# Kernel optimization log

Measured on AMD Instinct MI355X. Metric: run time of the kernel, lower is better.

## Reference

```python
import jax, jax.numpy as jnp
import numpy as np

ALPHA = 0.5      # dendritic temporal decay
BETA = 0.5       # somatic (LIF) decay
V_TH = 1.0
V_RESET = 0.0
N_COMP = 4       # B, dendritic compartments
SG_ALPHA = 4.0   # spikingjelly surrogate.Sigmoid default alpha


def mexican_hat(x, var=0.75, eps=1e-5):
    v = var + eps
    g = jnp.exp(-0.5 * x * x / v) / jnp.sqrt(2.0 * jnp.pi * v)
    return (1.0 - x * x / v) * g / v


@jax.custom_vjp
def heaviside_sg(x):
    # spikingjelly surrogate.Sigmoid: heaviside forward, sigmoid-derivative backward
    return (x >= 0.0).astype(x.dtype)

def _hs_fwd(x):
    return heaviside_sg(x), x

def _hs_bwd(x, g):
    s = jax.nn.sigmoid(SG_ALPHA * x)
    return (g * SG_ALPHA * s * (1.0 - s),)

heaviside_sg.defvjp(_hs_fwd, _hs_bwd)


def setup_inputs() -> dict:
    key = jax.random.key(0)
    k1, _ = jax.random.split(key)
    x_seq = jax.random.normal(k1, (8, 16, 128, 32, 32), dtype=jnp.float32)
    k = jnp.ones((1, N_COMP, 1), dtype=jnp.float32)  # dendritic strength param
    return {"x_seq": x_seq, "k": k}


def reference(x_seq, k):
    T, N, C, H, W = x_seq.shape
    B = N_COMP
    K = C // B
    L = H * W
    x = x_seq.reshape(T, N, K, B, L)

    # lower-triangular alpha decay matrix: A[i, j] = alpha**(i-j) for j <= i
    idx = jnp.arange(T)
    d = idx[:, None] - idx[None, :]
    A = jnp.where(d >= 0, ALPHA ** jnp.maximum(d, 0).astype(x.dtype),
                  jnp.zeros((), x.dtype)).astype(x.dtype)

    # causal alpha-weighted temporal sum (same math as dense broadcast+sum)
    pre_act = jnp.einsum('ts,snkbl->tnkbl', A, x)  # [T,N,K,B,L]

    fs = jax.nn.softmax(k, axis=1)                  # [1,B,1], normalized strength
    y_seq = (fs * 3.0 * mexican_hat(pre_act)).sum(axis=3)  # [T,N,K,L]

    # LIF soma recurrence with hard reset
    def step(h, y_t):
        h = BETA * h + y_t
        spike = heaviside_sg(h - V_TH)
        h = (1.0 - spike) * h + spike * V_RESET
        return h, spike

    h0 = jnp.zeros((N, K, L), dtype=x.dtype)
    _, spike_seq = jax.lax.scan(step, h0, y_seq)    # [T,N,K,L]
    return spike_seq.reshape(T, N, K, H, W)
```

## Files before the change

### kernel.cpp

```cpp
#include <hip/hip_runtime.h>


#define TT 8
#define NB 16
#define CC 128
#define BB 4
#define KK 32
#define LL 1024

__global__ __launch_bounds__(256) void dendsn_fwd(
    const float* __restrict__ x, const float* __restrict__ k,
    float* __restrict__ out)
{
    const int gid = blockIdx.x * 256 + threadIdx.x;
    const int l4 = gid & 255;
    const int kk = (gid >> 8) & 31;
    const int n  = gid >> 13;

    const float k0 = k[0], k1 = k[1], k2 = k[2], k3 = k[3];
    const float m  = fmaxf(fmaxf(k0, k1), fmaxf(k2, k3));
    const float e0 = expf(k0 - m), e1 = expf(k1 - m),
                e2 = expf(k2 - m), e3 = expf(k3 - m);
    const float inv_s = 1.0f / (e0 + e1 + e2 + e3);
    const float fs[4] = { 3.0f * e0 * inv_s, 3.0f * e1 * inv_s,
                          3.0f * e2 * inv_s, 3.0f * e3 * inv_s };

    const float v     = 0.75f + 1e-5f;
    const float inv_v = 1.0f / v;
    const float gs    = 1.0f / sqrtf(2.0f * 3.14159265358979323846f * v);

    const size_t tstride_x = (size_t)NB * CC * LL;
    const size_t tstride_o = (size_t)NB * KK * LL;
    const size_t base_x = ((size_t)n * CC + (size_t)kk * BB) * LL + (size_t)l4 * 4;
    const size_t base_o = ((size_t)n * KK + kk) * LL + (size_t)l4 * 4;

    float pre[4][4];
    float h[4];
    #pragma unroll
    for (int b = 0; b < 4; ++b)
        #pragma unroll
        for (int j = 0; j < 4; ++j) pre[b][j] = 0.0f;
    #pragma unroll
    for (int j = 0; j < 4; ++j) h[j] = 0.0f;

    for (int t = 0; t < TT; ++t) {
        float4 xv[4];
        #pragma unroll
        for (int b = 0; b < 4; ++b)
            xv[b] = *reinterpret_cast<const float4*>(
                        x + base_x + (size_t)t * tstride_x + (size_t)b * LL);

        float y[4] = {0.0f, 0.0f, 0.0f, 0.0f};
        #pragma unroll
        for (int b = 0; b < 4; ++b) {
            const float xs[4] = { xv[b].x, xv[b].y, xv[b].z, xv[b].w };
            #pragma unroll
            for (int j = 0; j < 4; ++j) {
                const float p = 0.5f * pre[b][j] + xs[j];
                pre[b][j] = p;
                const float q = p * p * inv_v;
                const float g = expf(-0.5f * q) * gs;
                y[j] += fs[b] * ((1.0f - q) * g * inv_v);
            }
        }

        float4 o;
        float* op = &o.x;
        #pragma unroll
        for (int j = 0; j < 4; ++j) {
            const float hh = 0.5f * h[j] + y[j];
            const float s  = (hh - 1.0f >= 0.0f) ? 1.0f : 0.0f;
            h[j] = (s != 0.0f) ? 0.0f : hh;
            op[j] = s;
        }
        *reinterpret_cast<float4*>(out + base_o + (size_t)t * tstride_o) = o;
    }
}

extern "C" void kernel_launch(void* const* d_in, const int* in_sizes, int n_in,
                              void* d_out, int out_size, void* d_ws, size_t ws_size,
                              hipStream_t stream)
{
    const float* x = (const float*)d_in[0];
    const float* k = (const float*)d_in[1];
    float* out = (float*)d_out;

    dendsn_fwd<<<512, 256, 0, stream>>>(x, k, out);
}
```

Measured before the change: 21.71 us.

## Split dendritic compartments across wave halves with shuffle reduction and prefetch

Each output quad is now handled by two lanes of a wavefront, each covering two of the four compartments, and the partial sums are combined with a cross-half shuffle. This doubles the thread count and the grid size, giving more waves in flight for a memory-bound kernel. It also software-prefetches the next timestep's inputs, fully unrolls the time loop and adds an occupancy hint to launch bounds. The cost is redundant LIF arithmetic in both halves, the shuffles, and only half of the lanes doing stores.

```diff
diff --git a/kernel.cpp b/kernel.cpp
--- a/kernel.cpp
+++ b/kernel.cpp
@@ -8,22 +8,30 @@
 #define KK 32
 #define LL 1024
 
-__global__ __launch_bounds__(256) void dendsn_fwd(
+__global__ __launch_bounds__(256, 4) void dendsn_fwd(
     const float* __restrict__ x, const float* __restrict__ k,
     float* __restrict__ out)
 {
-    const int gid = blockIdx.x * 256 + threadIdx.x;
-    const int l4 = gid & 255;
-    const int kk = (gid >> 8) & 31;
-    const int n  = gid >> 13;
+    const int tid  = threadIdx.x;
+    const int lane = tid & 63;
+    const int wv   = tid >> 6;
+    const int half = lane >> 5;
+    const int sl   = lane & 31;
+
+    const int pairIdx = (blockIdx.x * 4 + wv) * 32 + sl;
+    const int l4 = pairIdx & 255;
+    const int kk = (pairIdx >> 8) & 31;
+    const int n  = pairIdx >> 13;
+    const int b0 = half * 2;
 
     const float k0 = k[0], k1 = k[1], k2 = k[2], k3 = k[3];
     const float m  = fmaxf(fmaxf(k0, k1), fmaxf(k2, k3));
     const float e0 = expf(k0 - m), e1 = expf(k1 - m),
                 e2 = expf(k2 - m), e3 = expf(k3 - m);
     const float inv_s = 1.0f / (e0 + e1 + e2 + e3);
-    const float fs[4] = { 3.0f * e0 * inv_s, 3.0f * e1 * inv_s,
-                          3.0f * e2 * inv_s, 3.0f * e3 * inv_s };
+    const float fsa[4] = { 3.0f * e0 * inv_s, 3.0f * e1 * inv_s,
+                           3.0f * e2 * inv_s, 3.0f * e3 * inv_s };
+    const float fs0 = fsa[b0], fs1 = fsa[b0 + 1];
 
     const float v     = 0.75f + 1e-5f;
     const float inv_v = 1.0f / v;
@@ -31,38 +39,51 @@
 
     const size_t tstride_x = (size_t)NB * CC * LL;
     const size_t tstride_o = (size_t)NB * KK * LL;
-    const size_t base_x = ((size_t)n * CC + (size_t)kk * BB) * LL + (size_t)l4 * 4;
+    const size_t base_x = ((size_t)n * CC + (size_t)kk * BB + b0) * LL
+                        + (size_t)l4 * 4;
     const size_t base_o = ((size_t)n * KK + kk) * LL + (size_t)l4 * 4;
 
-    float pre[4][4];
+    float pre[2][4];
     float h[4];
     #pragma unroll
-    for (int b = 0; b < 4; ++b)
+    for (int b = 0; b < 2; ++b)
         #pragma unroll
         for (int j = 0; j < 4; ++j) pre[b][j] = 0.0f;
     #pragma unroll
     for (int j = 0; j < 4; ++j) h[j] = 0.0f;
 
+    float4 xv[2], xn[2];
+    xv[0] = *reinterpret_cast<const float4*>(x + base_x);
+    xv[1] = *reinterpret_cast<const float4*>(x + base_x + LL);
+
+    #pragma unroll
     for (int t = 0; t < TT; ++t) {
-        float4 xv[4];
+        if (t + 1 < TT) {
+            const size_t bx = base_x + (size_t)(t + 1) * tstride_x;
+            xn[0] = *reinterpret_cast<const float4*>(x + bx);
+            xn[1] = *reinterpret_cast<const float4*>(x + bx + LL);
+        }
+
+        float y[4];
         #pragma unroll
-        for (int b = 0; b < 4; ++b)
-            xv[b] = *reinterpret_cast<const float4*>(
-                        x + base_x + (size_t)t * tstride_x + (size_t)b * LL);
-
-        float y[4] = {0.0f, 0.0f, 0.0f, 0.0f};
+        for (int j = 0; j < 4; ++j) y[j] = 0.0f;
         #pragma unroll
-        for (int b = 0; b < 4; ++b) {
+        for (int b = 0; b < 2; ++b) {
             const float xs[4] = { xv[b].x, xv[b].y, xv[b].z, xv[b].w };
+            const float fsb = (b == 0) ? fs0 : fs1;
             #pragma unroll
             for (int j = 0; j < 4; ++j) {
                 const float p = 0.5f * pre[b][j] + xs[j];
                 pre[b][j] = p;
                 const float q = p * p * inv_v;
                 const float g = expf(-0.5f * q) * gs;
-                y[j] += fs[b] * ((1.0f - q) * g * inv_v);
+                y[j] += fsb * ((1.0f - q) * g * inv_v);
             }
         }
+
+        #pragma unroll
+        for (int j = 0; j < 4; ++j)
+            y[j] += __shfl_xor(y[j], 32);
 
         float4 o;
         float* op = &o.x;
@@ -73,7 +94,11 @@
             h[j] = (s != 0.0f) ? 0.0f : hh;
             op[j] = s;
         }
-        *reinterpret_cast<float4*>(out + base_o + (size_t)t * tstride_o) = o;
+        if (half == 0)
+            *reinterpret_cast<float4*>(out + base_o + (size_t)t * tstride_o) = o;
+
+        xv[0] = xn[0];
+        xv[1] = xn[1];
     }
 }
 
@@ -85,5 +110,5 @@
     const float* k = (const float*)d_in[1];
     float* out = (float*)d_out;
 
-    dendsn_fwd<<<512, 256, 0, stream>>>(x, k, out);
+    dendsn_fwd<<<1024, 256, 0, stream>>>(x, k, out);
 }
```

Measured after the change: 19.78 us, median of 3. 8.9% less time.

## Split dendritic compartments across wavefront lanes with shuffle reduction and prefetch

Applied to the files above, without the earlier changes.

Each thread now handles one dendritic compartment for 4 spatial sites instead of all four compartments, giving 4x more threads. The per-compartment contributions are summed with cross-lane xor shuffles, and only lanes with b==0 store the output. The next timestep's input load is software-prefetched and the time loop is fully unrolled. This raises parallelism and memory-level concurrency for a bandwidth-bound kernel, at the cost of redundant LIF work in 3/4 of the lanes and shuffle overhead.

```diff
diff --git a/kernel.cpp b/kernel.cpp
--- a/kernel.cpp
+++ b/kernel.cpp
@@ -8,22 +8,28 @@
 #define KK 32
 #define LL 1024
 
-__global__ __launch_bounds__(256) void dendsn_fwd(
+__global__ __launch_bounds__(256, 8) void dendsn_fwd(
     const float* __restrict__ x, const float* __restrict__ k,
     float* __restrict__ out)
 {
-    const int gid = blockIdx.x * 256 + threadIdx.x;
-    const int l4 = gid & 255;
-    const int kk = (gid >> 8) & 31;
-    const int n  = gid >> 13;
+    const int tid  = threadIdx.x;
+    const int lane = tid & 63;
+    const int b    = lane >> 4;
+    const int slot = lane & 15;
+
+    const int w     = (blockIdx.x * 256 + tid) >> 6;
+    const int site4 = w * 16 + slot;
+    const int l4 = site4 & 255;
+    const int kk = (site4 >> 8) & 31;
+    const int n  = site4 >> 13;
 
     const float k0 = k[0], k1 = k[1], k2 = k[2], k3 = k[3];
     const float m  = fmaxf(fmaxf(k0, k1), fmaxf(k2, k3));
     const float e0 = expf(k0 - m), e1 = expf(k1 - m),
                 e2 = expf(k2 - m), e3 = expf(k3 - m);
     const float inv_s = 1.0f / (e0 + e1 + e2 + e3);
-    const float fs[4] = { 3.0f * e0 * inv_s, 3.0f * e1 * inv_s,
-                          3.0f * e2 * inv_s, 3.0f * e3 * inv_s };
+    const float eb  = (b == 0) ? e0 : (b == 1) ? e1 : (b == 2) ? e2 : e3;
+    const float fsb = 3.0f * eb * inv_s;
 
     const float v     = 0.75f + 1e-5f;
     const float inv_v = 1.0f / v;
@@ -31,37 +37,40 @@
 
     const size_t tstride_x = (size_t)NB * CC * LL;
     const size_t tstride_o = (size_t)NB * KK * LL;
-    const size_t base_x = ((size_t)n * CC + (size_t)kk * BB) * LL + (size_t)l4 * 4;
+    const size_t base_x = ((size_t)n * CC + (size_t)kk * BB + b) * LL
+                        + (size_t)l4 * 4;
     const size_t base_o = ((size_t)n * KK + kk) * LL + (size_t)l4 * 4;
 
-    float pre[4][4];
+    float pre[4];
     float h[4];
     #pragma unroll
-    for (int b = 0; b < 4; ++b)
+    for (int j = 0; j < 4; ++j) { pre[j] = 0.0f; h[j] = 0.0f; }
+
+    float4 xv, xn;
+    xv = *reinterpret_cast<const float4*>(x + base_x);
+
+    #pragma unroll
+    for (int t = 0; t < TT; ++t) {
+        if (t + 1 < TT) {
+            xn = *reinterpret_cast<const float4*>(
+                     x + base_x + (size_t)(t + 1) * tstride_x);
+        }
+
+        const float xs[4] = { xv.x, xv.y, xv.z, xv.w };
+        float y[4];
         #pragma unroll
-        for (int j = 0; j < 4; ++j) pre[b][j] = 0.0f;
-    #pragma unroll
-    for (int j = 0; j < 4; ++j) h[j] = 0.0f;
+        for (int j = 0; j < 4; ++j) {
+            const float p = 0.5f * pre[j] + xs[j];
+            pre[j] = p;
+            const float q = p * p * inv_v;
+            const float g = expf(-0.5f * q) * gs;
+            y[j] = fsb * ((1.0f - q) * g * inv_v);
+        }
 
-    for (int t = 0; t < TT; ++t) {
-        float4 xv[4];
         #pragma unroll
-        for (int b = 0; b < 4; ++b)
-            xv[b] = *reinterpret_cast<const float4*>(
-                        x + base_x + (size_t)t * tstride_x + (size_t)b * LL);
-
-        float y[4] = {0.0f, 0.0f, 0.0f, 0.0f};
-        #pragma unroll
-        for (int b = 0; b < 4; ++b) {
-            const float xs[4] = { xv[b].x, xv[b].y, xv[b].z, xv[b].w };
-            #pragma unroll
-            for (int j = 0; j < 4; ++j) {
-                const float p = 0.5f * pre[b][j] + xs[j];
-                pre[b][j] = p;
-                const float q = p * p * inv_v;
-                const float g = expf(-0.5f * q) * gs;
-                y[j] += fs[b] * ((1.0f - q) * g * inv_v);
-            }
+        for (int j = 0; j < 4; ++j) {
+            y[j] += __shfl_xor(y[j], 16);
+            y[j] += __shfl_xor(y[j], 32);
         }
 
         float4 o;
@@ -73,7 +82,10 @@
             h[j] = (s != 0.0f) ? 0.0f : hh;
             op[j] = s;
         }
-        *reinterpret_cast<float4*>(out + base_o + (size_t)t * tstride_o) = o;
+        if (b == 0)
+            *reinterpret_cast<float4*>(out + base_o + (size_t)t * tstride_o) = o;
+
+        xv = xn;
     }
 }
 
@@ -85,5 +97,5 @@
     const float* k = (const float*)d_in[1];
     float* out = (float*)d_out;
 
-    dendsn_fwd<<<512, 256, 0, stream>>>(x, k, out);
+    dendsn_fwd<<<2048, 256, 0, stream>>>(x, k, out);
 }
```

Result: faster. 21.11 us (-2.8%).

## Map one spatial site per thread with next-timestep prefetch and more blocks

Applied to the files above, without the earlier changes.

Each thread now handles a single spatial element instead of four, and the grid grows four-fold to keep the total work the same. Inputs for the next timestep are loaded one iteration early, the time loop is fully unrolled, and launch bounds request higher occupancy. This aims to hide memory latency through more resident waves and software prefetch. In exchange it gives up 128-bit vector loads and stores for scalar accesses, which are still coalesced.

```diff
diff --git a/kernel.cpp b/kernel.cpp
--- a/kernel.cpp
+++ b/kernel.cpp
@@ -8,14 +8,14 @@
 #define KK 32
 #define LL 1024
 
-__global__ __launch_bounds__(256) void dendsn_fwd(
+__global__ __launch_bounds__(256, 8) void dendsn_fwd(
     const float* __restrict__ x, const float* __restrict__ k,
     float* __restrict__ out)
 {
-    const int gid = blockIdx.x * 256 + threadIdx.x;
-    const int l4 = gid & 255;
-    const int kk = (gid >> 8) & 31;
-    const int n  = gid >> 13;
+    const int site = blockIdx.x * 256 + threadIdx.x;
+    const int l  = site & 1023;
+    const int kk = (site >> 10) & 31;
+    const int n  = site >> 15;
 
     const float k0 = k[0], k1 = k[1], k2 = k[2], k3 = k[3];
     const float m  = fmaxf(fmaxf(k0, k1), fmaxf(k2, k3));
@@ -31,49 +31,43 @@
 
     const size_t tstride_x = (size_t)NB * CC * LL;
     const size_t tstride_o = (size_t)NB * KK * LL;
-    const size_t base_x = ((size_t)n * CC + (size_t)kk * BB) * LL + (size_t)l4 * 4;
-    const size_t base_o = ((size_t)n * KK + kk) * LL + (size_t)l4 * 4;
+    const size_t base_x = ((size_t)n * CC + (size_t)kk * BB) * LL + l;
+    const size_t base_o = ((size_t)n * KK + kk) * LL + l;
 
-    float pre[4][4];
-    float h[4];
+    float pre[4];
+    float h = 0.0f;
     #pragma unroll
-    for (int b = 0; b < 4; ++b)
-        #pragma unroll
-        for (int j = 0; j < 4; ++j) pre[b][j] = 0.0f;
+    for (int b = 0; b < 4; ++b) pre[b] = 0.0f;
+
+    float xv[4], xn[4];
     #pragma unroll
-    for (int j = 0; j < 4; ++j) h[j] = 0.0f;
+    for (int b = 0; b < 4; ++b) xv[b] = x[base_x + (size_t)b * LL];
 
+    #pragma unroll
     for (int t = 0; t < TT; ++t) {
-        float4 xv[4];
-        #pragma unroll
-        for (int b = 0; b < 4; ++b)
-            xv[b] = *reinterpret_cast<const float4*>(
-                        x + base_x + (size_t)t * tstride_x + (size_t)b * LL);
+        if (t + 1 < TT) {
+            const size_t bx = base_x + (size_t)(t + 1) * tstride_x;
+            #pragma unroll
+            for (int b = 0; b < 4; ++b) xn[b] = x[bx + (size_t)b * LL];
+        }
 
-        float y[4] = {0.0f, 0.0f, 0.0f, 0.0f};
+        float y = 0.0f;
         #pragma unroll
         for (int b = 0; b < 4; ++b) {
-            const float xs[4] = { xv[b].x, xv[b].y, xv[b].z, xv[b].w };
-            #pragma unroll
-            for (int j = 0; j < 4; ++j) {
-                const float p = 0.5f * pre[b][j] + xs[j];
-                pre[b][j] = p;
-                const float q = p * p * inv_v;
-                const float g = expf(-0.5f * q) * gs;
-                y[j] += fs[b] * ((1.0f - q) * g * inv_v);
-            }
+            const float p = 0.5f * pre[b] + xv[b];
+            pre[b] = p;
+            const float q = p * p * inv_v;
+            const float g = expf(-0.5f * q) * gs;
+            y += fs[b] * ((1.0f - q) * g * inv_v);
         }
 
-        float4 o;
-        float* op = &o.x;
+        const float hh = 0.5f * h + y;
+        const float s  = (hh - 1.0f >= 0.0f) ? 1.0f : 0.0f;
+        h = (s != 0.0f) ? 0.0f : hh;
+        out[base_o + (size_t)t * tstride_o] = s;
+
         #pragma unroll
-        for (int j = 0; j < 4; ++j) {
-            const float hh = 0.5f * h[j] + y[j];
-            const float s  = (hh - 1.0f >= 0.0f) ? 1.0f : 0.0f;
-            h[j] = (s != 0.0f) ? 0.0f : hh;
-            op[j] = s;
-        }
-        *reinterpret_cast<float4*>(out + base_o + (size_t)t * tstride_o) = o;
+        for (int b = 0; b < 4; ++b) xv[b] = xn[b];
     }
 }
 
@@ -85,5 +79,5 @@
     const float* k = (const float*)d_in[1];
     float* out = (float*)d_out;
 
-    dendsn_fwd<<<512, 256, 0, stream>>>(x, k, out);
+    dendsn_fwd<<<2048, 256, 0, stream>>>(x, k, out);
 }
```

Result: no change. 21.66 us (-0.2%).
